# Kernel tuning notes

Measured on AMD Instinct MI355X. Metric: run time of the kernel, lower is better.

The kernel has to match this reference:

```python
import jax, jax.numpy as jnp
import numpy as np

LEAKY = 0.2
BN_EPS = 1e-5
N_NODES = 50000
IN_F = 128
HID = 64
HEADS = 2
N_EDGES = 1600000


def _bn(x, gamma, beta):
    # BatchNorm1d in training mode: batch statistics over the node dim
    mu = jnp.mean(x, axis=0)
    var = jnp.mean((x - mu) ** 2, axis=0)
    return (x - mu) * jax.lax.rsqrt(var + BN_EPS) * gamma + beta


def _gat(x, src, dst, W, a_src, a_dst, bias, n):
    # W: [F_in, H*F], a_src/a_dst: [H, F]
    H, F = a_src.shape
    h = (x @ W).reshape(n, H, F)                      # [N,H,F]
    es = jnp.einsum('nhf,hf->nh', h, a_src)           # [N,H]
    ed = jnp.einsum('nhf,hf->nh', h, a_dst)           # [N,H]
    e = jax.nn.leaky_relu(es[src] + ed[dst], LEAKY)   # [E,H]
    m = jax.ops.segment_max(e, dst, num_segments=n)   # stable softmax per dst
    p = jnp.exp(e - m[dst])
    s = jax.ops.segment_sum(p, dst, num_segments=n)
    alpha = p / s[dst]                                # [E,H]
    out = jax.ops.segment_sum(h[src] * alpha[:, :, None], dst, num_segments=n)
    return out.reshape(n, H * F) + bias


def setup_inputs() -> dict:
    key = jax.random.key(0)
    ks = jax.random.split(key, 32)
    HF = HID * HEADS  # 128

    def g(k, shape, scale=0.1):
        return jax.random.normal(k, shape, dtype=jnp.float32) * scale

    inp = {
        'x': jax.random.normal(ks[0], (N_NODES, IN_F), dtype=jnp.float32),
        'edge_index': jax.random.randint(ks[1], (2, N_EDGES), 0, N_NODES, dtype=jnp.int64),
        # layer 1
        'W1': g(ks[2], (IN_F, HF)), 'as1': g(ks[3], (HEADS, HID)), 'ad1': g(ks[4], (HEADS, HID)),
        'gb1': jnp.zeros((HF,), jnp.float32),
        'lw1': g(ks[5], (IN_F, HF)), 'lb1': jnp.zeros((HF,), jnp.float32),
        'bg1': jnp.ones((IN_F,), jnp.float32), 'bb1': jnp.zeros((IN_F,), jnp.float32),
        # layer 2
        'W2': g(ks[6], (HF, HF)), 'as2': g(ks[7], (HEADS, HID)), 'ad2': g(ks[8], (HEADS, HID)),
        'gb2': jnp.zeros((HF,), jnp.float32),
        'lw2': g(ks[9], (HF, HF)), 'lb2': jnp.zeros((HF,), jnp.float32),
        'bg2': jnp.ones((HF,), jnp.float32), 'bb2': jnp.zeros((HF,), jnp.float32),
        # layer 3 (heads=1, out=2)
        'W3': g(ks[10], (HF, 2)), 'as3': g(ks[11], (1, 2)), 'ad3': g(ks[12], (1, 2)),
        'gb3': jnp.zeros((2,), jnp.float32),
        'lw3': g(ks[13], (HF, 2)), 'lb3': jnp.zeros((2,), jnp.float32),
        'bg3': jnp.ones((HF,), jnp.float32), 'bb3': jnp.zeros((HF,), jnp.float32),
    }
    return inp


def reference(x, edge_index,
              W1, as1, ad1, gb1, lw1, lb1, bg1, bb1,
              W2, as2, ad2, gb2, lw2, lb2, bg2, bb2,
              W3, as3, ad3, gb3, lw3, lb3, bg3, bb3):
    n = x.shape[0]
    loop = jnp.arange(n, dtype=edge_index.dtype)  # self-loops (PyG GAT default)
    src = jnp.concatenate([edge_index[0], loop])
    dst = jnp.concatenate([edge_index[1], loop])

    h = _bn(x, bg1, bb1)
    h = jax.nn.relu(h @ lw1 + lb1 + _gat(h, src, dst, W1, as1, ad1, gb1, n))
    h = _bn(h, bg2, bb2)
    h = jax.nn.relu(h @ lw2 + lb2 + _gat(h, src, dst, W2, as2, ad2, gb2, n))
    h = _bn(h, bg3, bb3)
    h = jax.nn.relu(h @ lw3 + lb3 + _gat(h, src, dst, W3, as3, ad3, gb3, n))
    return h
```

## Files before the change

kernel.cpp:

```cpp
#include <hip/hip_runtime.h>

#define LEAKY 0.2f
#define BN_EPS 1e-5f
#define BCHUNK 8192

typedef __bf16 v8bf __attribute__((ext_vector_type(8)));
typedef float v16f __attribute__((ext_vector_type(16)));
typedef float v2f __attribute__((ext_vector_type(2)));

__device__ __forceinline__ float wsum(float v) {
#pragma unroll
  for (int o = 32; o > 0; o >>= 1) v += __shfl_xor(v, o, 64);
  return v;
}

__device__ __forceinline__ float blo(unsigned u) { return __uint_as_float(u << 16); }
__device__ __forceinline__ float bhi(unsigned u) { return __uint_as_float(u & 0xffff0000u); }
__device__ __forceinline__ v2f bpair(unsigned u) {
  v2f r; r.x = __uint_as_float(u << 16); r.y = __uint_as_float(u & 0xffff0000u); return r;
}
__device__ __forceinline__ unsigned pack_bf16(float a, float b) {
  unsigned ua = __float_as_uint(a), ub = __float_as_uint(b);
  ua = (ua + 0x7fffu + ((ua >> 16) & 1u)) >> 16;
  ub = (ub + 0x7fffu + ((ub >> 16) & 1u)) >> 16;
  return ua | (ub << 16);
}
__device__ __forceinline__ unsigned short bf16of(float a) {
  unsigned ua = __float_as_uint(a);
  return (unsigned short)((ua + 0x7fffu + ((ua >> 16) & 1u)) >> 16);
}

__device__ __forceinline__ float dot2bf(unsigned a, unsigned b, float c) {
  asm("v_dot2_f32_bf16 %0, %1, %2, %0" : "+v"(c) : "v"(a), "v"(b));
  return c;
}
__device__ __forceinline__ unsigned permlo(unsigned u1, unsigned u2) {
  return __builtin_amdgcn_perm(u2, u1, 0x05040100u);
}
__device__ __forceinline__ unsigned permhi(unsigned u1, unsigned u2) {
  return __builtin_amdgcn_perm(u2, u1, 0x07060302u);
}

__device__ __forceinline__ int edge_at(const void* ei, int is64, long long i) {
  return is64 ? (int)((const long long*)ei)[i] : ((const int*)ei)[i];
}


__device__ __forceinline__ void binA_body(int blk, const void* ei, int N, int E, int M,
                                          int nb, int nblk, int* counts, int* lds) {
  int* hist = lds;
  int* sflag = lds + 1024;
  int tid = threadIdx.x;
  if (tid < 64) {
    const long long* p = (const long long*)ei;
    long long v = p[tid];
    int bad = (v < 0 || v >= (long long)N) ? 1 : 0;
    unsigned long long mres = __ballot(bad);
    if (tid == 0) *sflag = (mres == 0ull) ? 1 : 0;
  }
  for (int j = tid; j < nb; j += 256) hist[j] = 0;
  __syncthreads();
  int is64 = *sflag;
  long long base = (long long)blk * BCHUNK;
  int cnt = (int)min((long long)BCHUNK, (long long)M - base);
  for (int i = tid; i < cnt; i += 256) {
    long long g = base + i;
    int d = (g < E) ? edge_at(ei, is64, (long long)E + g) : (int)(g - E);
    atomicAdd(&hist[d >> 7], 1);
  }
  __syncthreads();
  for (int j = tid; j < nb; j += 256) counts[(size_t)j * nblk + blk] = hist[j];
}

__device__ __forceinline__ void binC_body(int blk, const void* ei, int N, int E, int M,
                                          int nb, int nblk, const int* counts,
                                          unsigned* tmp, int* lds) {
  int* cur = lds;
  int* sflag = lds + 1024;
  int tid = threadIdx.x;
  if (tid < 64) {
    const long long* p = (const long long*)ei;
    long long v = p[tid];
    int bad = (v < 0 || v >= (long long)N) ? 1 : 0;
    unsigned long long mres = __ballot(bad);
    if (tid == 0) *sflag = (mres == 0ull) ? 1 : 0;
  }
  for (int j = tid; j < nb; j += 256) cur[j] = counts[(size_t)j * nblk + blk];
  __syncthreads();
  int is64 = *sflag;
  long long base = (long long)blk * BCHUNK;
  int cnt = (int)min((long long)BCHUNK, (long long)M - base);
  for (int i = tid; i < cnt; i += 256) {
    long long g = base + i;
    int s, d;
    if (g < E) { s = edge_at(ei, is64, g); d = edge_at(ei, is64, (long long)E + g); }
    else       { s = d = (int)(g - E); }
    int pos = atomicAdd(&cur[d >> 7], 1);
    tmp[pos] = ((unsigned)s << 7) | (unsigned)(d & 127);
  }
}

#define MM_SMEM (32 * 136 * 2 + 128 * 4 + 128 * 4)

__device__ __forceinline__ void mm_body(int blk, const void* xin, int packed,
    const float* stats, const float* gamma, const float* beta,
    const unsigned short* Bp, unsigned* hb, unsigned* linp,
    float* es, float* ed, int N, char* smem) {
  unsigned short* Al = (unsigned short*)smem;
  float* scl_s = (float*)(smem + 8704);
  float* sht_s = (float*)(smem + 8704 + 512);
  int tid = threadIdx.x;
  int lane = tid & 63;
  int w = tid >> 6;
  int rowBase = blk * 32;

  if (tid < 128) {
    float s = 0.f, s2 = 0.f;
#pragma unroll
    for (int r = 0; r < 8; ++r) {
      s += stats[r * 256 + tid];
      s2 += stats[r * 256 + 128 + tid];
    }
    float inv_n = 1.0f / (float)N;
    float mu = s * inv_n;
    float var = s2 * inv_n - mu * mu;
    float rs = rsqrtf(var + BN_EPS);
    float sc = gamma[tid] * rs;
    scl_s[tid] = sc;
    sht_s[tid] = beta[tid] - mu * sc;
  }

  v8bf bfrag[2][8];
#pragma unroll
  for (int t = 0; t < 2; ++t)
#pragma unroll
    for (int s = 0; s < 8; ++s) {
      int fi = ((2 * w + t) * 8 + s) * 64 + lane;
      bfrag[t][s] = *(const v8bf*)&Bp[(size_t)fi * 8];
    }
  __syncthreads();

  if (!packed) {
    const float* x = (const float*)xin;
    for (int q = tid; q < 32 * 32; q += 256) {
      int r = q >> 5, k4 = (q & 31) * 4;
      int row = rowBase + r;
      float4 v = make_float4(0.f, 0.f, 0.f, 0.f);
      if (row < N) v = *(const float4*)&x[(size_t)row * 128 + k4];
      unsigned p0 = pack_bf16(v.x * scl_s[k4] + sht_s[k4], v.y * scl_s[k4 + 1] + sht_s[k4 + 1]);
      unsigned p1 = pack_bf16(v.z * scl_s[k4 + 2] + sht_s[k4 + 2], v.w * scl_s[k4 + 3] + sht_s[k4 + 3]);
      *(uint2*)&Al[r * 136 + k4] = make_uint2(p0, p1);
    }
  } else {
    const unsigned* xp = (const unsigned*)xin;
    for (int q = tid; q < 32 * 16; q += 256) {
      int r = q >> 4, g = q & 15;
      int row = rowBase + r;
      uint4 u = make_uint4(0u, 0u, 0u, 0u);
      if (row < N) u = *(const uint4*)&xp[(size_t)row * 64 + g * 4];
      int f = g * 8;
      uint4 o;
      o.x = pack_bf16(blo(u.x) * scl_s[f] + sht_s[f], bhi(u.x) * scl_s[f + 1] + sht_s[f + 1]);
      o.y = pack_bf16(blo(u.y) * scl_s[f + 2] + sht_s[f + 2], bhi(u.y) * scl_s[f + 3] + sht_s[f + 3]);
      o.z = pack_bf16(blo(u.z) * scl_s[f + 4] + sht_s[f + 4], bhi(u.z) * scl_s[f + 5] + sht_s[f + 5]);
      o.w = pack_bf16(blo(u.w) * scl_s[f + 6] + sht_s[f + 6], bhi(u.w) * scl_s[f + 7] + sht_s[f + 7]);
      *(uint4*)&Al[r * 136 + f] = o;
    }
  }
  __syncthreads();

  int m = lane & 31, half = lane >> 5;
  v8bf afrag[8];
#pragma unroll
  for (int s = 0; s < 8; ++s)
    afrag[s] = *(const v8bf*)&Al[m * 136 + s * 16 + half * 8];

  v16f acc0 = {}, acc1 = {};
#pragma unroll
  for (int s = 0; s < 8; ++s) {
    acc0 = __builtin_amdgcn_mfma_f32_32x32x16_bf16(afrag[s], bfrag[0][s], acc0, 0, 0, 0);
    acc1 = __builtin_amdgcn_mfma_f32_32x32x16_bf16(afrag[s], bfrag[1][s], acc1, 0, 0, 0);
  }

  v16f acc2 = {};
  if (w == 0) {
#pragma unroll
    for (int s = 0; s < 8; ++s) {
      v8bf besf = *(const v8bf*)&Bp[(size_t)((64 + s) * 64 + lane) * 8];
      acc2 = __builtin_amdgcn_mfma_f32_32x32x16_bf16(afrag[s], besf, acc2, 0, 0, 0);
    }
  }

  int mlo = half * 4;
  int t0 = 2 * w, t1 = 2 * w + 1;
#pragma unroll
  for (int r = 0; r < 16; ++r) {
    int row = (r & 3) + 8 * (r >> 2) + mlo;
    int node = rowBase + row;
    float a0 = acc0[r], a1 = acc1[r];
    float b0 = __shfl_xor(a0, 1, 64);
    float b1 = __shfl_xor(a1, 1, 64);
    if (node < N && !(lane & 1)) {
      if (t0 < 4) {
        hb[(size_t)node * 64 + (t0 * 16 + (m >> 1))] = pack_bf16(a0, b0);
        hb[(size_t)node * 64 + (t1 * 16 + (m >> 1))] = pack_bf16(a1, b1);
      } else {
        linp[(size_t)node * 64 + ((t0 - 4) * 16 + (m >> 1))] = pack_bf16(a0, b0);
        linp[(size_t)node * 64 + ((t1 - 4) * 16 + (m >> 1))] = pack_bf16(a1, b1);
      }
    }
    if (w == 0 && m < 4 && node < N) {
      float v = acc2[r];
      if (m < 2) es[2 * node + (m & 1)] = v;
      else       ed[2 * node + (m & 1)] = v;
    }
  }
}


__global__ __launch_bounds__(256) void k_prepA(
    const float* __restrict__ W1, const float* __restrict__ LW1,
    const float* __restrict__ W2, const float* __restrict__ LW2,
    const float* __restrict__ as1, const float* __restrict__ ad1,
    const float* __restrict__ as2, const float* __restrict__ ad2,
    const float* __restrict__ x, int N,
    unsigned short* __restrict__ Bp1, unsigned short* __restrict__ Bp2,
    float* __restrict__ stats1,
    const void* ei, int E, int M, int nb, int nblk, int* counts) {
  __shared__ __align__(16) int lds[1025];
  int blk = blockIdx.x;
  int tid = threadIdx.x;
  if (blk >= 1058) { binA_body(blk - 1058, ei, N, E, M, nb, nblk, counts, lds); return; }
  if (blk >= 34) {
    int b = blk - 34;
    int f = tid & 127;
    int half = tid >> 7;
    float s = 0.f, s2 = 0.f;
    for (int r = b + half * 1024; r < N; r += 2048) {
      float v = x[(size_t)r * 128 + f];
      s += v; s2 += v * v;
    }
    float* rep = stats1 + (size_t)(b & 7) * 256;
    atomicAdd(&rep[f], s);
    atomicAdd(&rep[128 + f], s2);
    return;
  }
  if (blk >= 32) {
    float (*wes)[4] = (float(*)[4])lds;
    const float* W = (blk == 32) ? W1 : W2;
    const float* as_ = (blk == 32) ? as1 : as2;
    const float* ad_ = (blk == 32) ? ad1 : ad2;
    unsigned short* Bp = (blk == 32) ? Bp1 : Bp2;
#pragma unroll
    for (int it = 0; it < 2; ++it) {
      int k = tid & 127;
      int c = (tid >> 7) + 2 * it;
      const float* a = (c < 2) ? as_ : ad_;
      int hb2 = (c & 1) * 64;
      float sum = 0.f;
      for (int f = 0; f < 64; ++f) sum += W[k * 128 + hb2 + f] * a[hb2 + f];
      wes[k][c] = sum;
    }
    __syncthreads();
    for (int fr = tid; fr < 512; fr += 256) {
      int lane = fr & 63, s = fr >> 6;
      int n = lane & 31;
      int k0 = s * 16 + (lane >> 5) * 8;
      unsigned short tb[8];
#pragma unroll
      for (int j = 0; j < 8; ++j)
        tb[j] = bf16of((n < 4) ? wes[k0 + j][n] : 0.f);
      uint4 pk;
      pk.x = (unsigned)tb[0] | ((unsigned)tb[1] << 16);
      pk.y = (unsigned)tb[2] | ((unsigned)tb[3] << 16);
      pk.z = (unsigned)tb[4] | ((unsigned)tb[5] << 16);
      pk.w = (unsigned)tb[6] | ((unsigned)tb[7] << 16);
      int fi = (64 + s) * 64 + lane;
      *(uint4*)&Bp[(size_t)fi * 8] = pk;
    }
    return;
  }
  const float* W  = (blk < 16) ? W1 : W2;
  const float* LW = (blk < 16) ? LW1 : LW2;
  unsigned short* Bp = (blk < 16) ? Bp1 : Bp2;
  int fi = (blk & 15) * 256 + tid;
  int lane = fi & 63, s = (fi >> 6) & 7, t = fi >> 9;
  int n = t * 32 + (lane & 31);
  int k0 = s * 16 + (lane >> 5) * 8;
  unsigned short tb[8];
#pragma unroll
  for (int j = 0; j < 8; ++j) {
    int k = k0 + j;
    float v = (n < 128) ? W[k * 128 + n] : LW[k * 128 + (n - 128)];
    tb[j] = bf16of(v);
  }
  uint4 pk;
  pk.x = (unsigned)tb[0] | ((unsigned)tb[1] << 16);
  pk.y = (unsigned)tb[2] | ((unsigned)tb[3] << 16);
  pk.z = (unsigned)tb[4] | ((unsigned)tb[5] << 16);
  pk.w = (unsigned)tb[6] | ((unsigned)tb[7] << 16);
  *(uint4*)&Bp[(size_t)fi * 8] = pk;
}

__global__ __launch_bounds__(1024) void k_binScan(int* counts, int total_entries) {
  __shared__ int part[1024];
  int tid = threadIdx.x;
  int per = (total_entries + 1023) / 1024;
  int lo = tid * per;
  int hi = lo + per; if (hi > total_entries) hi = total_entries;
  int s = 0;
  int i = lo;
  for (; i + 8 <= hi; i += 8) {
    int c0 = counts[i], c1 = counts[i + 1], c2 = counts[i + 2], c3 = counts[i + 3];
    int c4 = counts[i + 4], c5 = counts[i + 5], c6 = counts[i + 6], c7 = counts[i + 7];
    s += ((c0 + c1) + (c2 + c3)) + ((c4 + c5) + (c6 + c7));
  }
  for (; i < hi; ++i) s += counts[i];
  part[tid] = s;
  __syncthreads();
  for (int off = 1; off < 1024; off <<= 1) {
    int add = (tid >= off) ? part[tid - off] : 0;
    __syncthreads();
    part[tid] += add;
    __syncthreads();
  }
  int run = (tid == 0) ? 0 : part[tid - 1];
  i = lo;
  for (; i + 8 <= hi; i += 8) {
    int c0 = counts[i], c1 = counts[i + 1], c2 = counts[i + 2], c3 = counts[i + 3];
    int c4 = counts[i + 4], c5 = counts[i + 5], c6 = counts[i + 6], c7 = counts[i + 7];
    counts[i] = run; run += c0;
    counts[i + 1] = run; run += c1;
    counts[i + 2] = run; run += c2;
    counts[i + 3] = run; run += c3;
    counts[i + 4] = run; run += c4;
    counts[i + 5] = run; run += c5;
    counts[i + 6] = run; run += c6;
    counts[i + 7] = run; run += c7;
  }
  for (; i < hi; ++i) {
    int c = counts[i];
    counts[i] = run;
    run += c;
  }
}

__global__ __launch_bounds__(256) void k_mmC(
    const void* __restrict__ xin, int packed,
    const float* __restrict__ stats, const float* __restrict__ gamma, const float* __restrict__ beta,
    const unsigned short* __restrict__ Bp,
    unsigned* __restrict__ hb, unsigned* __restrict__ linp,
    float* __restrict__ es, float* __restrict__ ed, int N, int gmm,
    const void* ei, int E, int M, int nb, int nblk, const int* counts, unsigned* tmp) {
  __shared__ __align__(16) char smem[MM_SMEM];
  int blk = blockIdx.x;
  if (blk < gmm) {
    mm_body(blk, xin, packed, stats, gamma, beta, Bp, hb, linp, es, ed, N, smem);
  } else {
    binC_body(blk - gmm, ei, N, E, M, nb, nblk, counts, tmp, (int*)smem);
  }
}

__global__ __launch_bounds__(256) void k_mm(
    const void* __restrict__ xin, int packed,
    const float* __restrict__ stats, const float* __restrict__ gamma, const float* __restrict__ beta,
    const unsigned short* __restrict__ Bp,
    unsigned* __restrict__ hb, unsigned* __restrict__ linp,
    float* __restrict__ es, float* __restrict__ ed, int N) {
  __shared__ __align__(16) char smem[MM_SMEM];
  mm_body(blockIdx.x, xin, packed, stats, gamma, beta, Bp, hb, linp, es, ed, N, smem);
}

__global__ __launch_bounds__(256) void k_binD(const unsigned* __restrict__ tmp,
                                              const int* __restrict__ counts,
                                              int nb, int nblk, int M, int N,
                                              int* __restrict__ rowptr, int* __restrict__ col) {
  __shared__ int scn[128];
  __shared__ int cur[128];
  int tid = threadIdx.x;
  int j = blockIdx.x;
  int base = counts[(size_t)j * nblk];
  int endv = (j + 1 < nb) ? counts[(size_t)(j + 1) * nblk] : M;
  int bc = endv - base;
  if (tid < 128) scn[tid] = 0;
  __syncthreads();
  for (int i = tid; i < bc; i += 256) atomicAdd(&scn[tmp[base + i] & 127], 1);
  __syncthreads();
  int v = (tid < 128) ? scn[tid] : 0;
  __syncthreads();
  for (int off = 1; off < 128; off <<= 1) {
    int add = (tid >= off && tid < 128) ? scn[tid - off] : 0;
    __syncthreads();
    if (tid < 128) scn[tid] += add;
    __syncthreads();
  }
  if (tid < 128) {
    int excl = scn[tid] - v;
    int d = (j << 7) + tid;
    if (d < N) rowptr[d] = base + excl;
    cur[tid] = base + excl;
  }
  __syncthreads();
  for (int i = tid; i < bc; i += 256) {
    unsigned w = tmp[base + i];
    int pos = atomicAdd(&cur[w & 127], 1);
    col[pos] = (int)(w >> 7);
  }
  if (j == nb - 1 && tid == 0) rowptr[N] = M;
}

__global__ __launch_bounds__(128) void k_bnstats(const unsigned* __restrict__ xp,
                                                 int N, float* sums) {
  int f = threadIdx.x;
  int q = f >> 1, hi = f & 1;
  float s = 0.f, s2 = 0.f;
  for (int r = blockIdx.x; r < N; r += gridDim.x) {
    unsigned u = xp[(size_t)r * 64 + q];
    float v = hi ? bhi(u) : blo(u);
    s += v; s2 += v * v;
  }
  float* rep = sums + (size_t)(blockIdx.x & 7) * 256;
  atomicAdd(&rep[f], s);
  atomicAdd(&rep[128 + f], s2);
}

__global__ __launch_bounds__(256) void k_agg(
    const int* __restrict__ rowptr, const int* __restrict__ col,
    const float* __restrict__ es, const float* __restrict__ ed,
    const unsigned* __restrict__ hb, const unsigned* __restrict__ linp,
    const float* __restrict__ lb, const float* __restrict__ gb,
    unsigned* __restrict__ xoutp, int N) {
  __shared__ unsigned short phb[4][2][64];
  __shared__ unsigned obuf[4][64];
  int lane = threadIdx.x & 63;
  int w = threadIdx.x >> 6;
  int d = blockIdx.x * 4 + w;
  if (d >= N) return;
  int start = rowptr[d], end = rowptr[d + 1];
  v2f edv = *(const v2f*)&ed[2 * d];
  int q = lane >> 4;
  int m = lane & 15;
  int head_hi = m >= 8;
  v2f zero = {0.f, 0.f};
  v2f lk = {LEAKY, LEAKY};

  v2f acc[4] = {zero, zero, zero, zero};
  v2f spv = zero;
  unsigned short* ph = &phb[w][0][0];
  unsigned* oo = obuf[w];
  int hoff = head_hi ? 64 : 0;

  for (int base = start; base < end; base += 64) {
    int cnt = end - base; if (cnt > 64) cnt = 64;
    {
      int valid = lane < cnt;
      int s = col[valid ? base + lane : base];
      v2f ev = *(const v2f*)&es[2 * s];
      v2f e = ev + edv;
      v2f le = __builtin_elementwise_max(e, zero) + lk * __builtin_elementwise_min(e, zero);
      v2f p; p.x = __expf(le.x); p.y = __expf(le.y);
      if (!valid) p = zero;
      spv += p;
      ph[lane] = bf16of(p.x);
      ph[64 + lane] = bf16of(p.y);
      oo[lane] = (unsigned)s * 64u;
    }
    int i = 0;
    for (; i + 16 <= cnt; i += 16) {
      int e1 = i + 2 * q;
      int e2 = i + 8 + 2 * q;
      unsigned fpA = *(const unsigned*)&ph[hoff + e1];
      unsigned fpB = *(const unsigned*)&ph[hoff + e2];
      uint2 oA = *(const uint2*)&oo[e1];
      uint2 oB = *(const uint2*)&oo[e2];
      uint4 u1 = *(const uint4*)&hb[(size_t)oA.x + m * 4];
      uint4 u2 = *(const uint4*)&hb[(size_t)oA.y + m * 4];
      uint4 u3 = *(const uint4*)&hb[(size_t)oB.x + m * 4];
      uint4 u4 = *(const uint4*)&hb[(size_t)oB.y + m * 4];
      acc[0].x = dot2bf(fpA, permlo(u1.x, u2.x), acc[0].x);
      acc[0].y = dot2bf(fpA, permhi(u1.x, u2.x), acc[0].y);
      acc[1].x = dot2bf(fpA, permlo(u1.y, u2.y), acc[1].x);
      acc[1].y = dot2bf(fpA, permhi(u1.y, u2.y), acc[1].y);
      acc[2].x = dot2bf(fpA, permlo(u1.z, u2.z), acc[2].x);
      acc[2].y = dot2bf(fpA, permhi(u1.z, u2.z), acc[2].y);
      acc[3].x = dot2bf(fpA, permlo(u1.w, u2.w), acc[3].x);
      acc[3].y = dot2bf(fpA, permhi(u1.w, u2.w), acc[3].y);
      acc[0].x = dot2bf(fpB, permlo(u3.x, u4.x), acc[0].x);
      acc[0].y = dot2bf(fpB, permhi(u3.x, u4.x), acc[0].y);
      acc[1].x = dot2bf(fpB, permlo(u3.y, u4.y), acc[1].x);
      acc[1].y = dot2bf(fpB, permhi(u3.y, u4.y), acc[1].y);
      acc[2].x = dot2bf(fpB, permlo(u3.z, u4.z), acc[2].x);
      acc[2].y = dot2bf(fpB, permhi(u3.z, u4.z), acc[2].y);
      acc[3].x = dot2bf(fpB, permlo(u3.w, u4.w), acc[3].x);
      acc[3].y = dot2bf(fpB, permhi(u3.w, u4.w), acc[3].y);
    }
    for (; i < cnt; i += 8) {
      int e1 = i + 2 * q;
      unsigned fp = *(const unsigned*)&ph[hoff + e1];
      uint2 ofs = *(const uint2*)&oo[e1];
      uint4 u1 = *(const uint4*)&hb[(size_t)ofs.x + m * 4];
      uint4 u2 = *(const uint4*)&hb[(size_t)ofs.y + m * 4];
      acc[0].x = dot2bf(fp, permlo(u1.x, u2.x), acc[0].x);
      acc[0].y = dot2bf(fp, permhi(u1.x, u2.x), acc[0].y);
      acc[1].x = dot2bf(fp, permlo(u1.y, u2.y), acc[1].x);
      acc[1].y = dot2bf(fp, permhi(u1.y, u2.y), acc[1].y);
      acc[2].x = dot2bf(fp, permlo(u1.z, u2.z), acc[2].x);
      acc[2].y = dot2bf(fp, permhi(u1.z, u2.z), acc[2].y);
      acc[3].x = dot2bf(fp, permlo(u1.w, u2.w), acc[3].x);
      acc[3].y = dot2bf(fp, permhi(u1.w, u2.w), acc[3].y);
    }
  }
#pragma unroll
  for (int k = 0; k < 4; ++k) {
    acc[k].x += __shfl_xor(acc[k].x, 16, 64);
    acc[k].x += __shfl_xor(acc[k].x, 32, 64);
    acc[k].y += __shfl_xor(acc[k].y, 16, 64);
    acc[k].y += __shfl_xor(acc[k].y, 32, 64);
  }
#pragma unroll
  for (int o = 1; o < 64; o <<= 1) {
    spv.x += __shfl_xor(spv.x, o, 64);
    spv.y += __shfl_xor(spv.y, o, 64);
  }

  if (q == 0) {
    float inv = 1.0f / (head_hi ? spv.y : spv.x);
    uint4 lv = *(const uint4*)&linp[(size_t)d * 64 + m * 4];
    int f8 = 8 * m;
    float4 lb0 = *(const float4*)&lb[f8], lb1 = *(const float4*)&lb[f8 + 4];
    float4 gb0 = *(const float4*)&gb[f8], gb1 = *(const float4*)&gb[f8 + 4];
    float v0 = blo(lv.x) + lb0.x + acc[0].x * inv + gb0.x;
    float v1 = bhi(lv.x) + lb0.y + acc[0].y * inv + gb0.y;
    float v2 = blo(lv.y) + lb0.z + acc[1].x * inv + gb0.z;
    float v3 = bhi(lv.y) + lb0.w + acc[1].y * inv + gb0.w;
    float v4 = blo(lv.z) + lb1.x + acc[2].x * inv + gb1.x;
    float v5 = bhi(lv.z) + lb1.y + acc[2].y * inv + gb1.y;
    float v6 = blo(lv.w) + lb1.z + acc[3].x * inv + gb1.z;
    float v7 = bhi(lv.w) + lb1.w + acc[3].y * inv + gb1.w;
    v0 = v0 > 0.f ? v0 : 0.f; v1 = v1 > 0.f ? v1 : 0.f;
    v2 = v2 > 0.f ? v2 : 0.f; v3 = v3 > 0.f ? v3 : 0.f;
    v4 = v4 > 0.f ? v4 : 0.f; v5 = v5 > 0.f ? v5 : 0.f;
    v6 = v6 > 0.f ? v6 : 0.f; v7 = v7 > 0.f ? v7 : 0.f;
    uint4 o;
    o.x = pack_bf16(v0, v1); o.y = pack_bf16(v2, v3);
    o.z = pack_bf16(v4, v5); o.w = pack_bf16(v6, v7);
    *(uint4*)&xoutp[(size_t)d * 64 + m * 4] = o;
  }
}

__global__ __launch_bounds__(256) void k_l3node(
    const unsigned* __restrict__ xp,
    const float* __restrict__ stats, const float* __restrict__ gamma, const float* __restrict__ beta,
    const float* __restrict__ W3, const float* __restrict__ LW3,
    const float* __restrict__ as3, const float* __restrict__ ad3,
    float* h3, float* lin3, float* es3, float* ed3, int N) {
  int lane = threadIdx.x & 63;
  int n = blockIdx.x * 4 + (threadIdx.x >> 6);
  if (n >= N) return;
  float inv_n = 1.0f / (float)N;
  int f0 = lane, f1 = 64 + lane;
  float su0 = 0.f, sq0 = 0.f, su1 = 0.f, sq1 = 0.f;
#pragma unroll
  for (int r = 0; r < 8; ++r) {
    su0 += stats[r * 256 + f0];  sq0 += stats[r * 256 + 128 + f0];
    su1 += stats[r * 256 + f1];  sq1 += stats[r * 256 + 128 + f1];
  }
  float mu0 = su0 * inv_n;
  float var0 = sq0 * inv_n - mu0 * mu0;
  float rs0 = rsqrtf(var0 + BN_EPS);
  float sc0 = gamma[f0] * rs0, sh0 = beta[f0] - mu0 * sc0;
  float mu1 = su1 * inv_n;
  float var1 = sq1 * inv_n - mu1 * mu1;
  float rs1 = rsqrtf(var1 + BN_EPS);
  float sc1 = gamma[f1] * rs1, sh1 = beta[f1] - mu1 * sc1;

  unsigned ua = xp[(size_t)n * 64 + (lane >> 1)];
  unsigned ub = xp[(size_t)n * 64 + 32 + (lane >> 1)];
  float xv0 = (lane & 1) ? bhi(ua) : blo(ua);
  float xv1 = (lane & 1) ? bhi(ub) : blo(ub);
  float xn0 = xv0 * sc0 + sh0;
  float xn1 = xv1 * sc1 + sh1;

  float2 w0 = *(const float2*)&W3[lane * 2];
  float2 w1 = *(const float2*)&W3[(64 + lane) * 2];
  float2 l0 = *(const float2*)&LW3[lane * 2];
  float2 l1 = *(const float2*)&LW3[(64 + lane) * 2];
  float hc0 = wsum(xn0 * w0.x + xn1 * w1.x);
  float hc1 = wsum(xn0 * w0.y + xn1 * w1.y);
  float lc0 = wsum(xn0 * l0.x + xn1 * l1.x);
  float lc1 = wsum(xn0 * l0.y + xn1 * l1.y);
  if (lane == 0) {
    h3[2 * n] = hc0; h3[2 * n + 1] = hc1;
    lin3[2 * n] = lc0; lin3[2 * n + 1] = lc1;
    es3[n] = hc0 * as3[0] + hc1 * as3[1];
    ed3[n] = hc0 * ad3[0] + hc1 * ad3[1];
  }
}

__global__ __launch_bounds__(256) void k_agg3(
    const int* __restrict__ rowptr, const int* __restrict__ col,
    const float* __restrict__ es, const float* __restrict__ ed,
    const float* __restrict__ h3, const float* __restrict__ lin3,
    const float* __restrict__ lb3, const float* __restrict__ gb3,
    float* __restrict__ out, int N) {
  int lane = threadIdx.x & 63;
  int d = blockIdx.x * 4 + (threadIdx.x >> 6);
  if (d >= N) return;
  int start = rowptr[d], end = rowptr[d + 1];
  float edd = ed[d];
  float ps = 0.f, a0 = 0.f, a1 = 0.f;
  for (int i = start + lane; i < end; i += 64) {
    int s = col[i];
    float e = es[s] + edd; e = e > 0.f ? e : LEAKY * e;
    float p = __expf(e);
    float2 hv = *(const float2*)&h3[2 * s];
    ps += p; a0 += p * hv.x; a1 += p * hv.y;
  }
  ps = wsum(ps); a0 = wsum(a0); a1 = wsum(a1);
  if (lane < 2) {
    float a = (lane == 0 ? a0 : a1) / ps;
    float v = lin3[2 * d + lane] + lb3[lane] + a + gb3[lane];
    out[2 * d + lane] = v > 0.f ? v : 0.f;
  }
}

extern "C" void kernel_launch(void* const* d_in, const int* in_sizes, int n_in,
                              void* d_out, int out_size, void* d_ws, size_t ws_size,
                              hipStream_t stream) {
  const float* x   = (const float*)d_in[0];
  const void*  ei  = d_in[1];
  const float* W1  = (const float*)d_in[2];
  const float* as1 = (const float*)d_in[3];
  const float* ad1 = (const float*)d_in[4];
  const float* gb1 = (const float*)d_in[5];
  const float* lw1 = (const float*)d_in[6];
  const float* lb1 = (const float*)d_in[7];
  const float* bg1 = (const float*)d_in[8];
  const float* bb1 = (const float*)d_in[9];
  const float* W2  = (const float*)d_in[10];
  const float* as2 = (const float*)d_in[11];
  const float* ad2 = (const float*)d_in[12];
  const float* gb2 = (const float*)d_in[13];
  const float* lw2 = (const float*)d_in[14];
  const float* lb2 = (const float*)d_in[15];
  const float* bg2 = (const float*)d_in[16];
  const float* bb2 = (const float*)d_in[17];
  const float* W3  = (const float*)d_in[18];
  const float* as3 = (const float*)d_in[19];
  const float* ad3 = (const float*)d_in[20];
  const float* gb3 = (const float*)d_in[21];
  const float* lw3 = (const float*)d_in[22];
  const float* lb3 = (const float*)d_in[23];
  const float* bg3 = (const float*)d_in[24];
  const float* bb3 = (const float*)d_in[25];
  float* out = (float*)d_out;

  int N = in_sizes[0] / 128;
  int E = in_sizes[1] / 2;
  int M = E + N;
  int nb = (N + 127) >> 7;
  int nblk = (M + BCHUNK - 1) / BCHUNK;

  char* wsp = (char*)d_ws;
  size_t off = 0;
  auto alloc = [&](size_t bytes) -> void* {
    void* p = wsp + off;
    off = (off + bytes + 255) & ~(size_t)255;
    return p;
  };
  int* rowptr   = (int*)alloc(((size_t)N + 1) * 4);
  int* col      = (int*)alloc((size_t)M * 4);
  unsigned* tmp = (unsigned*)alloc((size_t)M * 4);
  int* counts   = (int*)alloc(((size_t)nb * nblk + 1) * 4);
  float* st1    = (float*)alloc(8 * 256 * 4);
  float* st2    = (float*)alloc(8 * 256 * 4);
  float* st3    = (float*)alloc(8 * 256 * 4);
  unsigned short* Bp1 = (unsigned short*)alloc(4608 * 16);
  unsigned short* Bp2 = (unsigned short*)alloc(4608 * 16);
  unsigned* hbp  = (unsigned*)alloc((size_t)N * 64 * 4);
  unsigned* linp = (unsigned*)alloc((size_t)N * 64 * 4);
  unsigned* x2p  = (unsigned*)alloc((size_t)N * 64 * 4);
  float* es    = (float*)alloc((size_t)N * 2 * 4);
  float* edb   = (float*)alloc((size_t)N * 2 * 4);
  float* h3    = (float*)alloc((size_t)N * 2 * 4);
  float* lin3  = (float*)alloc((size_t)N * 2 * 4);
  float* es3   = (float*)alloc((size_t)N * 4);
  float* ed3   = (float*)alloc((size_t)N * 4);
  (void)ws_size; (void)n_in; (void)out_size;

  hipMemsetAsync(st1, 0, 3 * 8 * 256 * 4, stream);

  int gnode = (N + 3) / 4;
  int gmm = (N + 31) / 32;

  k_prepA<<<1058 + nblk, 256, 0, stream>>>(W1, lw1, W2, lw2, as1, ad1, as2, ad2,
                                           x, N, Bp1, Bp2, st1,
                                           ei, E, M, nb, nblk, counts);
  k_binScan<<<1, 1024, 0, stream>>>(counts, nb * nblk);
  k_mmC<<<gmm + nblk, 256, 0, stream>>>(x, 0, st1, bg1, bb1, Bp1, hbp, linp, es, edb, N,
                                        gmm, ei, E, M, nb, nblk, counts, tmp);
  k_binD<<<nb, 256, 0, stream>>>(tmp, counts, nb, nblk, M, N, rowptr, col);

  k_agg<<<gnode, 256, 0, stream>>>(rowptr, col, es, edb, hbp, linp, lb1, gb1, x2p, N);

  k_bnstats<<<1024, 128, 0, stream>>>(x2p, N, st2);
  k_mm<<<gmm, 256, 0, stream>>>(x2p, 1, st2, bg2, bb2, Bp2, hbp, linp, es, edb, N);
  k_agg<<<gnode, 256, 0, stream>>>(rowptr, col, es, edb, hbp, linp, lb2, gb2, x2p, N);

  k_bnstats<<<1024, 128, 0, stream>>>(x2p, N, st3);
  k_l3node<<<gnode, 256, 0, stream>>>(x2p, st3, bg3, bb3, W3, lw3, as3, ad3,
                                      h3, lin3, es3, ed3, N);
  k_agg3<<<gnode, 256, 0, stream>>>(rowptr, col, es3, ed3, h3, lin3, lb3, gb3, out, N);
}
```

Baseline: 428.4 us.

## Build CSR with direct global per-node atomics instead of two-level binning

```diff
diff --git a/kernel.cpp b/kernel.cpp
--- a/kernel.cpp
+++ b/kernel.cpp
@@ -46,10 +46,8 @@
 }
 
 
-__device__ __forceinline__ void binA_body(int blk, const void* ei, int N, int E, int M,
-                                          int nb, int nblk, int* counts, int* lds) {
-  int* hist = lds;
-  int* sflag = lds + 1024;
+__device__ __forceinline__ void histA_body(int blk, const void* ei, int N, int E, int M,
+                                           int* cnt, int* sflag) {
   int tid = threadIdx.x;
   if (tid < 64) {
     const long long* p = (const long long*)ei;
@@ -58,25 +56,19 @@
     unsigned long long mres = __ballot(bad);
     if (tid == 0) *sflag = (mres == 0ull) ? 1 : 0;
   }
-  for (int j = tid; j < nb; j += 256) hist[j] = 0;
   __syncthreads();
   int is64 = *sflag;
   long long base = (long long)blk * BCHUNK;
-  int cnt = (int)min((long long)BCHUNK, (long long)M - base);
-  for (int i = tid; i < cnt; i += 256) {
+  int c = (int)min((long long)BCHUNK, (long long)M - base);
+  for (int i = tid; i < c; i += 256) {
     long long g = base + i;
     int d = (g < E) ? edge_at(ei, is64, (long long)E + g) : (int)(g - E);
-    atomicAdd(&hist[d >> 7], 1);
-  }
-  __syncthreads();
-  for (int j = tid; j < nb; j += 256) counts[(size_t)j * nblk + blk] = hist[j];
-}
-
-__device__ __forceinline__ void binC_body(int blk, const void* ei, int N, int E, int M,
-                                          int nb, int nblk, const int* counts,
-                                          unsigned* tmp, int* lds) {
-  int* cur = lds;
-  int* sflag = lds + 1024;
+    atomicAdd(&cnt[d], 1);
+  }
+}
+
+__device__ __forceinline__ void scat_body(int blk, const void* ei, int N, int E, int M,
+                                          int* cur, int* col, int* sflag) {
   int tid = threadIdx.x;
   if (tid < 64) {
     const long long* p = (const long long*)ei;
@@ -85,18 +77,17 @@
     unsigned long long mres = __ballot(bad);
     if (tid == 0) *sflag = (mres == 0ull) ? 1 : 0;
   }
-  for (int j = tid; j < nb; j += 256) cur[j] = counts[(size_t)j * nblk + blk];
   __syncthreads();
   int is64 = *sflag;
   long long base = (long long)blk * BCHUNK;
-  int cnt = (int)min((long long)BCHUNK, (long long)M - base);
-  for (int i = tid; i < cnt; i += 256) {
+  int c = (int)min((long long)BCHUNK, (long long)M - base);
+  for (int i = tid; i < c; i += 256) {
     long long g = base + i;
     int s, d;
     if (g < E) { s = edge_at(ei, is64, g); d = edge_at(ei, is64, (long long)E + g); }
     else       { s = d = (int)(g - E); }
-    int pos = atomicAdd(&cur[d >> 7], 1);
-    tmp[pos] = ((unsigned)s << 7) | (unsigned)(d & 127);
+    int pos = atomicAdd(&cur[d], 1);
+    col[pos] = s;
   }
 }
 
@@ -226,11 +217,11 @@
     const float* __restrict__ x, int N,
     unsigned short* __restrict__ Bp1, unsigned short* __restrict__ Bp2,
     float* __restrict__ stats1,
-    const void* ei, int E, int M, int nb, int nblk, int* counts) {
+    const void* ei, int E, int M, int nblk, int* cnt) {
   __shared__ __align__(16) int lds[1025];
   int blk = blockIdx.x;
   int tid = threadIdx.x;
-  if (blk >= 1058) { binA_body(blk - 1058, ei, N, E, M, nb, nblk, counts, lds); return; }
+  if (blk >= 1058) { histA_body(blk - 1058, ei, N, E, M, cnt, lds + 1024); return; }
   if (blk >= 34) {
     int b = blk - 34;
     int f = tid & 127;
@@ -302,20 +293,16 @@
   *(uint4*)&Bp[(size_t)fi * 8] = pk;
 }
 
-__global__ __launch_bounds__(1024) void k_binScan(int* counts, int total_entries) {
+__global__ __launch_bounds__(1024) void k_binScan(const int* __restrict__ cnt, int Nn, int M,
+                                                  int* __restrict__ rowptr,
+                                                  int* __restrict__ cur) {
   __shared__ int part[1024];
   int tid = threadIdx.x;
-  int per = (total_entries + 1023) / 1024;
+  int per = (Nn + 1023) / 1024;
   int lo = tid * per;
-  int hi = lo + per; if (hi > total_entries) hi = total_entries;
+  int hi = lo + per; if (hi > Nn) hi = Nn;
   int s = 0;
-  int i = lo;
-  for (; i + 8 <= hi; i += 8) {
-    int c0 = counts[i], c1 = counts[i + 1], c2 = counts[i + 2], c3 = counts[i + 3];
-    int c4 = counts[i + 4], c5 = counts[i + 5], c6 = counts[i + 6], c7 = counts[i + 7];
-    s += ((c0 + c1) + (c2 + c3)) + ((c4 + c5) + (c6 + c7));
-  }
-  for (; i < hi; ++i) s += counts[i];
+  for (int i = lo; i < hi; ++i) s += cnt[i];
   part[tid] = s;
   __syncthreads();
   for (int off = 1; off < 1024; off <<= 1) {
@@ -325,24 +312,13 @@
     __syncthreads();
   }
   int run = (tid == 0) ? 0 : part[tid - 1];
-  i = lo;
-  for (; i + 8 <= hi; i += 8) {
-    int c0 = counts[i], c1 = counts[i + 1], c2 = counts[i + 2], c3 = counts[i + 3];
-    int c4 = counts[i + 4], c5 = counts[i + 5], c6 = counts[i + 6], c7 = counts[i + 7];
-    counts[i] = run; run += c0;
-    counts[i + 1] = run; run += c1;
-    counts[i + 2] = run; run += c2;
-    counts[i + 3] = run; run += c3;
-    counts[i + 4] = run; run += c4;
-    counts[i + 5] = run; run += c5;
-    counts[i + 6] = run; run += c6;
-    counts[i + 7] = run; run += c7;
-  }
-  for (; i < hi; ++i) {
-    int c = counts[i];
-    counts[i] = run;
+  for (int i = lo; i < hi; ++i) {
+    int c = cnt[i];
+    rowptr[i] = run;
+    cur[i] = run;
     run += c;
   }
+  if (tid == 1023) rowptr[Nn] = M;
 }
 
 __global__ __launch_bounds__(256) void k_mmC(
@@ -351,13 +327,13 @@
     const unsigned short* __restrict__ Bp,
     unsigned* __restrict__ hb, unsigned* __restrict__ linp,
     float* __restrict__ es, float* __restrict__ ed, int N, int gmm,
-    const void* ei, int E, int M, int nb, int nblk, const int* counts, unsigned* tmp) {
+    const void* ei, int E, int M, int nblk, int* cur, int* col) {
   __shared__ __align__(16) char smem[MM_SMEM];
   int blk = blockIdx.x;
   if (blk < gmm) {
     mm_body(blk, xin, packed, stats, gamma, beta, Bp, hb, linp, es, ed, N, smem);
   } else {
-    binC_body(blk - gmm, ei, N, E, M, nb, nblk, counts, tmp, (int*)smem);
+    scat_body(blk - gmm, ei, N, E, M, cur, col, (int*)smem);
   }
 }
 
@@ -369,44 +345,6 @@
     float* __restrict__ es, float* __restrict__ ed, int N) {
   __shared__ __align__(16) char smem[MM_SMEM];
   mm_body(blockIdx.x, xin, packed, stats, gamma, beta, Bp, hb, linp, es, ed, N, smem);
-}
-
-__global__ __launch_bounds__(256) void k_binD(const unsigned* __restrict__ tmp,
-                                              const int* __restrict__ counts,
-                                              int nb, int nblk, int M, int N,
-                                              int* __restrict__ rowptr, int* __restrict__ col) {
-  __shared__ int scn[128];
-  __shared__ int cur[128];
-  int tid = threadIdx.x;
-  int j = blockIdx.x;
-  int base = counts[(size_t)j * nblk];
-  int endv = (j + 1 < nb) ? counts[(size_t)(j + 1) * nblk] : M;
-  int bc = endv - base;
-  if (tid < 128) scn[tid] = 0;
-  __syncthreads();
-  for (int i = tid; i < bc; i += 256) atomicAdd(&scn[tmp[base + i] & 127], 1);
-  __syncthreads();
-  int v = (tid < 128) ? scn[tid] : 0;
-  __syncthreads();
-  for (int off = 1; off < 128; off <<= 1) {
-    int add = (tid >= off && tid < 128) ? scn[tid - off] : 0;
-    __syncthreads();
-    if (tid < 128) scn[tid] += add;
-    __syncthreads();
-  }
-  if (tid < 128) {
-    int excl = scn[tid] - v;
-    int d = (j << 7) + tid;
-    if (d < N) rowptr[d] = base + excl;
-    cur[tid] = base + excl;
-  }
-  __syncthreads();
-  for (int i = tid; i < bc; i += 256) {
-    unsigned w = tmp[base + i];
-    int pos = atomicAdd(&cur[w & 127], 1);
-    col[pos] = (int)(w >> 7);
-  }
-  if (j == nb - 1 && tid == 0) rowptr[N] = M;
 }
 
 __global__ __launch_bounds__(128) void k_bnstats(const unsigned* __restrict__ xp,
@@ -658,7 +596,6 @@
   int N = in_sizes[0] / 128;
   int E = in_sizes[1] / 2;
   int M = E + N;
-  int nb = (N + 127) >> 7;
   int nblk = (M + BCHUNK - 1) / BCHUNK;
 
   char* wsp = (char*)d_ws;
@@ -670,8 +607,8 @@
   };
   int* rowptr   = (int*)alloc(((size_t)N + 1) * 4);
   int* col      = (int*)alloc((size_t)M * 4);
-  unsigned* tmp = (unsigned*)alloc((size_t)M * 4);
-  int* counts   = (int*)alloc(((size_t)nb * nblk + 1) * 4);
+  int* cnt      = (int*)alloc((size_t)N * 4);
+  int* cur      = (int*)alloc((size_t)N * 4);
   float* st1    = (float*)alloc(8 * 256 * 4);
   float* st2    = (float*)alloc(8 * 256 * 4);
   float* st3    = (float*)alloc(8 * 256 * 4);
@@ -689,17 +626,17 @@
   (void)ws_size; (void)n_in; (void)out_size;
 
   hipMemsetAsync(st1, 0, 3 * 8 * 256 * 4, stream);
+  hipMemsetAsync(cnt, 0, (size_t)N * 4, stream);
 
   int gnode = (N + 3) / 4;
   int gmm = (N + 31) / 32;
 
   k_prepA<<<1058 + nblk, 256, 0, stream>>>(W1, lw1, W2, lw2, as1, ad1, as2, ad2,
                                            x, N, Bp1, Bp2, st1,
-                                           ei, E, M, nb, nblk, counts);
-  k_binScan<<<1, 1024, 0, stream>>>(counts, nb * nblk);
+                                           ei, E, M, nblk, cnt);
+  k_binScan<<<1, 1024, 0, stream>>>(cnt, N, M, rowptr, cur);
   k_mmC<<<gmm + nblk, 256, 0, stream>>>(x, 0, st1, bg1, bb1, Bp1, hbp, linp, es, edb, N,
-                                        gmm, ei, E, M, nb, nblk, counts, tmp);
-  k_binD<<<nb, 256, 0, stream>>>(tmp, counts, nb, nblk, M, N, rowptr, col);
+                                        gmm, ei, E, M, nblk, cur, col);
 
   k_agg<<<gnode, 256, 0, stream>>>(rowptr, col, es, edb, hbp, linp, lb1, gb1, x2p, N);
 
```

Measured after the change: 597.6 us. 1.39x slower.

## Split single-block bin count scan into per-bucket row scans plus bucket-base scan

Applied to the files above, without the earlier changes.

```diff
diff --git a/kernel.cpp b/kernel.cpp
--- a/kernel.cpp
+++ b/kernel.cpp
@@ -74,6 +74,7 @@
 
 __device__ __forceinline__ void binC_body(int blk, const void* ei, int N, int E, int M,
                                           int nb, int nblk, const int* counts,
+                                          const int* bucketBase,
                                           unsigned* tmp, int* lds) {
   int* cur = lds;
   int* sflag = lds + 1024;
@@ -85,7 +86,8 @@
     unsigned long long mres = __ballot(bad);
     if (tid == 0) *sflag = (mres == 0ull) ? 1 : 0;
   }
-  for (int j = tid; j < nb; j += 256) cur[j] = counts[(size_t)j * nblk + blk];
+  for (int j = tid; j < nb; j += 256)
+    cur[j] = bucketBase[j] + counts[(size_t)j * nblk + blk];
   __syncthreads();
   int is64 = *sflag;
   long long base = (long long)blk * BCHUNK;
@@ -302,47 +304,57 @@
   *(uint4*)&Bp[(size_t)fi * 8] = pk;
 }
 
-__global__ __launch_bounds__(1024) void k_binScan(int* counts, int total_entries) {
-  __shared__ int part[1024];
+__global__ __launch_bounds__(256) void k_scanA(int* __restrict__ counts, int nblk,
+                                               int* __restrict__ rowTotal) {
+  __shared__ int part[256];
   int tid = threadIdx.x;
-  int per = (total_entries + 1023) / 1024;
+  int j = blockIdx.x;
+  int* row = counts + (size_t)j * nblk;
+  int per = (nblk + 255) / 256;
   int lo = tid * per;
-  int hi = lo + per; if (hi > total_entries) hi = total_entries;
+  int hi = lo + per; if (hi > nblk) hi = nblk;
   int s = 0;
-  int i = lo;
-  for (; i + 8 <= hi; i += 8) {
-    int c0 = counts[i], c1 = counts[i + 1], c2 = counts[i + 2], c3 = counts[i + 3];
-    int c4 = counts[i + 4], c5 = counts[i + 5], c6 = counts[i + 6], c7 = counts[i + 7];
-    s += ((c0 + c1) + (c2 + c3)) + ((c4 + c5) + (c6 + c7));
-  }
-  for (; i < hi; ++i) s += counts[i];
+  for (int i = lo; i < hi; ++i) s += row[i];
   part[tid] = s;
   __syncthreads();
-  for (int off = 1; off < 1024; off <<= 1) {
+  for (int off = 1; off < 256; off <<= 1) {
     int add = (tid >= off) ? part[tid - off] : 0;
     __syncthreads();
     part[tid] += add;
     __syncthreads();
   }
   int run = (tid == 0) ? 0 : part[tid - 1];
-  i = lo;
-  for (; i + 8 <= hi; i += 8) {
-    int c0 = counts[i], c1 = counts[i + 1], c2 = counts[i + 2], c3 = counts[i + 3];
-    int c4 = counts[i + 4], c5 = counts[i + 5], c6 = counts[i + 6], c7 = counts[i + 7];
-    counts[i] = run; run += c0;
-    counts[i + 1] = run; run += c1;
-    counts[i + 2] = run; run += c2;
-    counts[i + 3] = run; run += c3;
-    counts[i + 4] = run; run += c4;
-    counts[i + 5] = run; run += c5;
-    counts[i + 6] = run; run += c6;
-    counts[i + 7] = run; run += c7;
-  }
-  for (; i < hi; ++i) {
-    int c = counts[i];
-    counts[i] = run;
+  for (int i = lo; i < hi; ++i) {
+    int c = row[i];
+    row[i] = run;
     run += c;
   }
+  if (tid == 0) rowTotal[j] = part[255];
+}
+
+__global__ __launch_bounds__(512) void k_scanB(const int* __restrict__ rowTotal, int nb,
+                                               int M, int* __restrict__ bucketBase) {
+  __shared__ int part[512];
+  int tid = threadIdx.x;
+  int per = (nb + 511) / 512;
+  int lo = tid * per;
+  int hi = lo + per; if (hi > nb) hi = nb;
+  int s = 0;
+  for (int i = lo; i < hi; ++i) s += rowTotal[i];
+  part[tid] = s;
+  __syncthreads();
+  for (int off = 1; off < 512; off <<= 1) {
+    int add = (tid >= off) ? part[tid - off] : 0;
+    __syncthreads();
+    part[tid] += add;
+    __syncthreads();
+  }
+  int run = (tid == 0) ? 0 : part[tid - 1];
+  for (int i = lo; i < hi; ++i) {
+    bucketBase[i] = run;
+    run += rowTotal[i];
+  }
+  if (tid == 0) bucketBase[nb] = M;
 }
 
 __global__ __launch_bounds__(256) void k_mmC(
@@ -351,13 +363,14 @@
     const unsigned short* __restrict__ Bp,
     unsigned* __restrict__ hb, unsigned* __restrict__ linp,
     float* __restrict__ es, float* __restrict__ ed, int N, int gmm,
-    const void* ei, int E, int M, int nb, int nblk, const int* counts, unsigned* tmp) {
+    const void* ei, int E, int M, int nb, int nblk, const int* counts,
+    const int* bucketBase, unsigned* tmp) {
   __shared__ __align__(16) char smem[MM_SMEM];
   int blk = blockIdx.x;
   if (blk < gmm) {
     mm_body(blk, xin, packed, stats, gamma, beta, Bp, hb, linp, es, ed, N, smem);
   } else {
-    binC_body(blk - gmm, ei, N, E, M, nb, nblk, counts, tmp, (int*)smem);
+    binC_body(blk - gmm, ei, N, E, M, nb, nblk, counts, bucketBase, tmp, (int*)smem);
   }
 }
 
@@ -372,15 +385,15 @@
 }
 
 __global__ __launch_bounds__(256) void k_binD(const unsigned* __restrict__ tmp,
-                                              const int* __restrict__ counts,
-                                              int nb, int nblk, int M, int N,
+                                              const int* __restrict__ bucketBase,
+                                              int nb, int M, int N,
                                               int* __restrict__ rowptr, int* __restrict__ col) {
   __shared__ int scn[128];
   __shared__ int cur[128];
   int tid = threadIdx.x;
   int j = blockIdx.x;
-  int base = counts[(size_t)j * nblk];
-  int endv = (j + 1 < nb) ? counts[(size_t)(j + 1) * nblk] : M;
+  int base = bucketBase[j];
+  int endv = bucketBase[j + 1];
   int bc = endv - base;
   if (tid < 128) scn[tid] = 0;
   __syncthreads();
@@ -672,6 +685,8 @@
   int* col      = (int*)alloc((size_t)M * 4);
   unsigned* tmp = (unsigned*)alloc((size_t)M * 4);
   int* counts   = (int*)alloc(((size_t)nb * nblk + 1) * 4);
+  int* rowTotal = (int*)alloc((size_t)nb * 4);
+  int* bucketBase = (int*)alloc(((size_t)nb + 1) * 4);
   float* st1    = (float*)alloc(8 * 256 * 4);
   float* st2    = (float*)alloc(8 * 256 * 4);
   float* st3    = (float*)alloc(8 * 256 * 4);
@@ -696,10 +711,11 @@
   k_prepA<<<1058 + nblk, 256, 0, stream>>>(W1, lw1, W2, lw2, as1, ad1, as2, ad2,
                                            x, N, Bp1, Bp2, st1,
                                            ei, E, M, nb, nblk, counts);
-  k_binScan<<<1, 1024, 0, stream>>>(counts, nb * nblk);
+  k_scanA<<<nb, 256, 0, stream>>>(counts, nblk, rowTotal);
+  k_scanB<<<1, 512, 0, stream>>>(rowTotal, nb, M, bucketBase);
   k_mmC<<<gmm + nblk, 256, 0, stream>>>(x, 0, st1, bg1, bb1, Bp1, hbp, linp, es, edb, N,
-                                        gmm, ei, E, M, nb, nblk, counts, tmp);
-  k_binD<<<nb, 256, 0, stream>>>(tmp, counts, nb, nblk, M, N, rowptr, col);
+                                        gmm, ei, E, M, nb, nblk, counts, bucketBase, tmp);
+  k_binD<<<nb, 256, 0, stream>>>(tmp, bucketBase, nb, M, N, rowptr, col);
 
   k_agg<<<gnode, 256, 0, stream>>>(rowptr, col, es, edb, hbp, linp, lb1, gb1, x2p, N);
 
```

New measurement: 394.7 us. 1.09x faster.
